# Optimization experiments

Measured on AMD Instinct MI355X. Metric: run time of the kernel, lower is better.

## Reference

```python
import jax, jax.numpy as jnp
import numpy as np

K = 4        # maximum_fertility + 1
OOV_ID = 1
HIDDEN = 512


def setup_inputs() -> dict:
    key = jax.random.key(0)
    ks = jax.random.split(key, 8)
    B, S, D, E, H, V = 4, 128, 512, 256, HIDDEN, 32000
    return {
        "embedded_input": jax.random.normal(ks[0], (B, S, D), jnp.float32),
        "input_mask": jnp.ones((B, S), jnp.int32),
        "emb_table": jax.random.normal(ks[1], (V, E), jnp.float32) * 0.02,
        "W_ih": jax.random.normal(ks[2], (4 * H, D + E), jnp.float32) * 0.02,
        "b_ih": jax.random.normal(ks[3], (4 * H,), jnp.float32) * 0.02,
        "W_hh": jax.random.normal(ks[4], (4 * H, H), jnp.float32) * 0.02,
        "b_hh": jax.random.normal(ks[5], (4 * H,), jnp.float32) * 0.02,
        "W_out": jax.random.normal(ks[6], (V, H), jnp.float32) * 0.02,
        "b_out": jax.random.normal(ks[7], (V,), jnp.float32) * 0.02,
    }


def reference(embedded_input, input_mask, emb_table, W_ih, b_ih, W_hh, b_hh, W_out, b_out):
    B, S, D = embedded_input.shape
    V, E = emb_table.shape
    H = HIDDEN
    N = B * S
    x = embedded_input.reshape(N, D)                      # (N, D)
    h0 = jnp.zeros((N, H), embedded_input.dtype)
    c0 = jnp.zeros((N, H), embedded_input.dtype)
    # initial last_output: one-hot at OOV id (prob mass 1.0 on oov)
    last0 = jnp.zeros((N, V), embedded_input.dtype).at[:, OOV_ID].set(1.0)

    def step(carry, _):
        h, c, last = carry
        # embedding_bag soft mix over full vocab == weighted sum == matmul
        emb_last = last @ emb_table                        # (N, E)
        inp = jnp.concatenate([x, emb_last], axis=1)       # (N, D+E)
        gates = inp @ W_ih.T + b_ih + h @ W_hh.T + b_hh    # (N, 4H)
        i, f, g, o = jnp.split(gates, 4, axis=1)           # torch LSTMCell gate order
        i = jax.nn.sigmoid(i)
        f = jax.nn.sigmoid(f)
        g = jnp.tanh(g)
        o = jax.nn.sigmoid(o)
        c_new = f * c + i * g
        h_new = o * jnp.tanh(c_new)
        # dropout=0 / eval -> dropout mask is all ones (no-op)
        logits = h_new @ W_out.T + b_out                   # (N, V)
        logp = jax.nn.log_softmax(logits, axis=-1)
        return (h_new, c_new, jnp.exp(logp)), logp

    _, outs = jax.lax.scan(step, (h0, c0, last0), None, length=K)  # (K, N, V)
    return outs.transpose(1, 0, 2).reshape(B, S, K, V)
```

## Files before the change

### kernel.cpp

```cpp
#include <hip/hip_runtime.h>
#include <hip/hip_bf16.h>
#include <math.h>

#define N_ROWS 512
#define D_IN   512
#define E_EMB  256
#define H_DIM  512
#define G_DIM  2048
#define V_DIM  32000
#define IN_LD  1280
#define K_STEPS 4
#define OOV_ID 1
#define TBK 64
#define EMB_SPLIT 50
#define EMB_CHUNK 640
#define SEGSTRIDE 512

typedef __attribute__((ext_vector_type(4))) float f32x4;
typedef __attribute__((ext_vector_type(8))) short bf16x8;
typedef __attribute__((ext_vector_type(8))) _Float16 f16x8;

__device__ inline short f2b(float v) {
    __hip_bfloat16 h = __float2bfloat16(v);
    return *reinterpret_cast<short*>(&h);
}

__device__ inline void gload_lds(const short* g, short* l) {
    __builtin_amdgcn_global_load_lds(
        (const __attribute__((address_space(1))) void*)g,
        (__attribute__((address_space(3))) void*)l, 16, 0, 0);
}

template<int TBM, int TBN, int WR_, int WC_, int MODE>
__global__ __launch_bounds__(WR_ * WC_ * 64) void k_gemm(
    const short* __restrict__ A, int lda,
    const short* __restrict__ B, int ldb,
    const float* __restrict__ bias,
    float* __restrict__ C, size_t ldc, int Kc,
    float2* __restrict__ stats,
    float* __restrict__ cstate, short* __restrict__ hdst,
    float* __restrict__ outdst, size_t ldout, const float* __restrict__ lsep)
{
    constexpr int NW = WR_ * WC_;
    constexpr int WMT = TBM / WR_, WNT = TBN / WC_;
    constexpr int WM = WMT / 16, WN = WNT / 16;
    __shared__ short As[TBM * 64];
    __shared__ short Bs[TBN * 64];
    const int tid = threadIdx.x;
    const int lane = tid & 63, wid = tid >> 6;
    const int wr = wid % WR_, wc = wid / WR_;
    const int quad = lane >> 4, l16 = lane & 15;
    const int m0 = blockIdx.y * TBM, n0 = blockIdx.x * TBN;
    const int kbase = blockIdx.z * Kc;
    const int lrow = lane >> 3;
    const int lsw  = ((lane & 7) ^ lrow) * 8;

    f32x4 acc[WM][WN];
#pragma unroll
    for (int i = 0; i < WM; ++i)
#pragma unroll
        for (int j = 0; j < WN; ++j)
#pragma unroll
            for (int r = 0; r < 4; ++r) acc[i][j][r] = 0.0f;

    for (int kt = 0; kt < Kc; kt += TBK) {
        const int k0 = kbase + kt;
        if constexpr (MODE == 5) {
#pragma unroll
            for (int ch = wid; ch < TBN / 8; ch += NW)
                gload_lds(&B[(size_t)(n0 + ch * 8 + lrow) * ldb + k0 + lsw], &Bs[ch * 512]);
            const _Float16* Z = (const _Float16*)A;
#pragma unroll
            for (int ch = wid; ch < TBM / 8; ch += NW) {
                const int row = m0 + ch * 8 + lrow;
                const int col = k0 + lsw;
                f16x8 zv = *(const f16x8*)&Z[(size_t)row * lda + col];
                const float l = lsep[row];
                float lp[8];
#pragma unroll
                for (int q = 0; q < 8; ++q) lp[q] = (float)zv[q] - l;
                float4* od = (float4*)&outdst[(size_t)row * ldout + col];
                od[0] = make_float4(lp[0], lp[1], lp[2], lp[3]);
                od[1] = make_float4(lp[4], lp[5], lp[6], lp[7]);
                bf16x8 p;
#pragma unroll
                for (int q = 0; q < 8; ++q) p[q] = f2b(__expf(lp[q]));
                *(bf16x8*)&As[ch * 512 + lane * 8] = p;
            }
        } else {
#pragma unroll
            for (int ch = wid; ch < TBM / 8; ch += NW)
                gload_lds(&A[(size_t)(m0 + ch * 8 + lrow) * lda + k0 + lsw], &As[ch * 512]);
#pragma unroll
            for (int ch = wid; ch < TBN / 8; ch += NW)
                gload_lds(&B[(size_t)(n0 + ch * 8 + lrow) * ldb + k0 + lsw], &Bs[ch * 512]);
        }
        __syncthreads();
#pragma unroll
        for (int ks = 0; ks < 2; ++ks) {
            bf16x8 af[WM], bfv[WN];
#pragma unroll
            for (int i = 0; i < WM; ++i) {
                int rr = wr * WMT + i * 16 + l16;
                af[i] = *(const bf16x8*)&As[rr * 64 + (((ks * 4 + quad) ^ (l16 & 7)) * 8)];
            }
#pragma unroll
            for (int j = 0; j < WN; ++j) {
                int rr = wc * WNT + j * 16 + l16;
                bfv[j] = *(const bf16x8*)&Bs[rr * 64 + (((ks * 4 + quad) ^ (l16 & 7)) * 8)];
            }
#pragma unroll
            for (int i = 0; i < WM; ++i)
#pragma unroll
                for (int j = 0; j < WN; ++j)
                    acc[i][j] = __builtin_amdgcn_mfma_f32_16x16x32_bf16(af[i], bfv[j], acc[i][j], 0, 0, 0);
        }
        __syncthreads();
    }

    if constexpr (MODE == 3 || MODE == 5) {
        float* Cp = C + (size_t)blockIdx.z * N_ROWS * ldc;
#pragma unroll
        for (int i = 0; i < WM; ++i)
#pragma unroll
            for (int j = 0; j < WN; ++j) {
                const int n = n0 + wc * WNT + j * 16 + l16;
#pragma unroll
                for (int r = 0; r < 4; ++r) {
                    const int m = m0 + wr * WMT + i * 16 + quad * 4 + r;
                    Cp[(size_t)m * ldc + n] = acc[i][j][r];
                }
            }
    } else if constexpr (MODE == 2) {
        float bv[WN];
#pragma unroll
        for (int j = 0; j < WN; ++j) bv[j] = bias[n0 + j * 16 + l16];
        const int jj = (n0 >> 2) + l16;
#pragma unroll
        for (int i = 0; i < WM; ++i) {
#pragma unroll
            for (int r = 0; r < 4; ++r) {
                const int m = m0 + wr * WMT + i * 16 + quad * 4 + r;
                float gi = acc[i][0][r] + bv[0];
                float gf = acc[i][1][r] + bv[1];
                float gg = acc[i][2][r] + bv[2];
                float go = acc[i][3][r] + bv[3];
                float i_ = 1.0f / (1.0f + expf(-gi));
                float f_ = 1.0f / (1.0f + expf(-gf));
                float g_ = tanhf(gg);
                float o_ = 1.0f / (1.0f + expf(-go));
                const size_t ci = (size_t)m * H_DIM + jj;
                float cn = f_ * cstate[ci] + i_ * g_;
                cstate[ci] = cn;
                hdst[(size_t)m * IN_LD + (D_IN + E_EMB) + jj] = f2b(o_ * tanhf(cn));
            }
        }
    } else if constexpr (MODE == 4) {
        _Float16* Ch = (_Float16*)C;
        float bv[WN];
#pragma unroll
        for (int j = 0; j < WN; ++j) bv[j] = bias[n0 + wc * WNT + j * 16 + l16];
#pragma unroll
        for (int i = 0; i < WM; ++i) {
            float rm[4] = {-1e30f, -1e30f, -1e30f, -1e30f};
            float rs[4] = {0.f, 0.f, 0.f, 0.f};
#pragma unroll
            for (int j = 0; j < WN; ++j)
#pragma unroll
                for (int r = 0; r < 4; ++r)
                    rm[r] = fmaxf(rm[r], acc[i][j][r] + bv[j]);
#pragma unroll
            for (int j = 0; j < WN; ++j) {
                const int n = n0 + wc * WNT + j * 16 + l16;
#pragma unroll
                for (int r = 0; r < 4; ++r) {
                    const int m = m0 + wr * WMT + i * 16 + quad * 4 + r;
                    float z = acc[i][j][r] + bv[j];
                    rs[r] += __expf(z - rm[r]);
                    Ch[(size_t)m * ldc + n] = (_Float16)z;
                }
            }
#pragma unroll
            for (int mask = 1; mask < 16; mask <<= 1) {
#pragma unroll
                for (int r = 0; r < 4; ++r) {
                    float om = __shfl_xor(rm[r], mask);
                    float os = __shfl_xor(rs[r], mask);
                    float nm = fmaxf(rm[r], om);
                    rs[r] = rs[r] * __expf(rm[r] - nm) + os * __expf(om - nm);
                    rm[r] = nm;
                }
            }
            if (l16 == 0) {
                const int seg = (n0 + wc * WNT) >> 6;
#pragma unroll
                for (int r = 0; r < 4; ++r) {
                    const int m = m0 + wr * WMT + i * 16 + quad * 4 + r;
                    stats[(size_t)m * SEGSTRIDE + seg] = make_float2(rm[r], rs[r]);
                }
            }
        }
    } else {
        float bv[WN];
#pragma unroll
        for (int j = 0; j < WN; ++j) bv[j] = bias[n0 + wc * WNT + j * 16 + l16];
#pragma unroll
        for (int i = 0; i < WM; ++i)
#pragma unroll
            for (int j = 0; j < WN; ++j) {
                const int n = n0 + wc * WNT + j * 16 + l16;
#pragma unroll
                for (int r = 0; r < 4; ++r) {
                    const int m = m0 + wr * WMT + i * 16 + quad * 4 + r;
                    C[(size_t)m * ldc + n] = acc[i][j][r] + bv[j];
                }
            }
    }
}

__global__ __launch_bounds__(256) void k_prep(
    const float* __restrict__ x, const float* __restrict__ emb_table,
    const float* __restrict__ W_ih, const float* __restrict__ W_hh,
    const float* __restrict__ b_ih, const float* __restrict__ b_hh,
    const float* __restrict__ W_out,
    short* __restrict__ Abuf, short* __restrict__ Wg, float* __restrict__ bsum,
    short* __restrict__ Wout16, float* __restrict__ c)
{
    const int idx0 = blockIdx.x * 256 + threadIdx.x;
    const int gs = gridDim.x * 256;
    const float4* W4 = (const float4*)W_out;
    for (int i = idx0; i < V_DIM * H_DIM / 4; i += gs) {
        float4 v = W4[i];
        short4 o;
        o.x = f2b(v.x); o.y = f2b(v.y); o.z = f2b(v.z); o.w = f2b(v.w);
        ((short4*)Wout16)[i] = o;
    }
    for (int i = idx0; i < G_DIM * IN_LD; i += gs) {
        int rp = i / IN_LD, k = i - rp * IN_LD;
        int j = ((rp >> 6) << 4) | (rp & 15);
        int gate = (rp >> 4) & 3;
        int g = gate * H_DIM + j;
        float v = (k < D_IN + E_EMB) ? W_ih[(size_t)g * (D_IN + E_EMB) + k]
                                     : W_hh[(size_t)g * H_DIM + (k - (D_IN + E_EMB))];
        Wg[i] = f2b(v);
    }
    for (int i = idx0; i < G_DIM; i += gs) {
        int j = ((i >> 6) << 4) | (i & 15);
        int gate = (i >> 4) & 3;
        int g = gate * H_DIM + j;
        bsum[i] = b_ih[g] + b_hh[g];
    }
    for (int i = idx0; i < N_ROWS * IN_LD; i += gs) {
        int n = i / IN_LD, col = i - n * IN_LD;
        float v;
        if (col < D_IN)              v = x[(size_t)n * D_IN + col];
        else if (col < D_IN + E_EMB) v = emb_table[(size_t)OOV_ID * E_EMB + (col - D_IN)];
        else                         v = 0.0f;
        Abuf[i] = f2b(v);
    }
    for (int i = idx0; i < N_ROWS * H_DIM; i += gs) c[i] = 0.0f;
}

__global__ __launch_bounds__(256) void k_trans(const float* __restrict__ emb,
                                               short* __restrict__ embT)
{
    __shared__ float tile[64][65];
    const int v0 = blockIdx.x * 64, e0 = blockIdx.y * 64;
    const int tid = threadIdx.x;
#pragma unroll
    for (int i = 0; i < 16; ++i) {
        int idx = tid + i * 256;
        int vr = idx >> 6, ec = idx & 63;
        tile[vr][ec] = emb[(size_t)(v0 + vr) * E_EMB + e0 + ec];
    }
    __syncthreads();
#pragma unroll
    for (int i = 0; i < 16; ++i) {
        int idx = tid + i * 256;
        int er = idx >> 6, vc = idx & 63;
        embT[(size_t)(e0 + er) * V_DIM + v0 + vc] = f2b(tile[vc][er]);
    }
}

__global__ __launch_bounds__(256) void k_embred(const float* __restrict__ ep,
                                                short* __restrict__ Abuf)
{
    int idx = blockIdx.x * 256 + threadIdx.x;
    int n = idx >> 8, e = idx & 255;
    float s0 = 0.f, s1 = 0.f;
#pragma unroll 2
    for (int z = 0; z < EMB_SPLIT; z += 2) {
        s0 += ep[((size_t)z * N_ROWS + n) * E_EMB + e];
        s1 += ep[((size_t)(z + 1) * N_ROWS + n) * E_EMB + e];
    }
    Abuf[(size_t)n * IN_LD + D_IN + e] = f2b(s0 + s1);
}

__global__ __launch_bounds__(256) void k_lse(const float2* __restrict__ stats,
                                             float* __restrict__ lse)
{
    const int tid = threadIdx.x;
    const int lane = tid & 63, wid = tid >> 6;
    const int n = blockIdx.x * 4 + wid;

    float m = -1e30f, s = 0.0f;
    for (int sg = lane; sg < V_DIM / 64; sg += 64) {
        float2 p = stats[(size_t)n * SEGSTRIDE + sg];
        float nm = fmaxf(m, p.x);
        s = s * __expf(m - nm) + p.y * __expf(p.x - nm);
        m = nm;
    }
#pragma unroll
    for (int mask = 32; mask > 0; mask >>= 1) {
        float om = __shfl_xor(m, mask);
        float os = __shfl_xor(s, mask);
        float nm = fmaxf(m, om);
        s = s * __expf(m - nm) + os * __expf(om - nm);
        m = nm;
    }
    if (lane == 0) lse[n] = m + __logf(s);
}

__global__ __launch_bounds__(256) void k_finish(const _Float16* __restrict__ zbuf,
                                                float* __restrict__ out,
                                                const float* __restrict__ lse,
                                                int step)
{
    const int n = blockIdx.y;
    const float l = lse[n];
    const f16x8* zr = (const f16x8*)(zbuf + (size_t)n * V_DIM);
    float4* row4 = (float4*)(out + ((size_t)n * K_STEPS + step) * V_DIM);
#pragma unroll
    for (int it = 0; it < 2; ++it) {
        const int slot = threadIdx.x + it * 256;
        if (slot < 500) {
            const int cidx = blockIdx.x * 500 + slot;
            f16x8 zv = zr[cidx];
            float lp[8];
#pragma unroll
            for (int k = 0; k < 8; ++k) lp[k] = (float)zv[k] - l;
            row4[cidx * 2]     = make_float4(lp[0], lp[1], lp[2], lp[3]);
            row4[cidx * 2 + 1] = make_float4(lp[4], lp[5], lp[6], lp[7]);
        }
    }
}

extern "C" void kernel_launch(void* const* d_in, const int* in_sizes, int n_in,
                              void* d_out, int out_size, void* d_ws, size_t ws_size,
                              hipStream_t stream) {
    (void)in_sizes; (void)n_in; (void)out_size; (void)ws_size;
    const float* x       = (const float*)d_in[0];
    const float* emb_tab = (const float*)d_in[2];
    const float* W_ih    = (const float*)d_in[3];
    const float* b_ih    = (const float*)d_in[4];
    const float* W_hh    = (const float*)d_in[5];
    const float* b_hh    = (const float*)d_in[6];
    const float* W_out   = (const float*)d_in[7];
    const float* b_out   = (const float*)d_in[8];
    float* out = (float*)d_out;

    char* ws = (char*)d_ws;
    short* Abuf   = (short*)ws;  ws += (size_t)N_ROWS * IN_LD * sizeof(short);
    float* c      = (float*)ws;  ws += (size_t)N_ROWS * H_DIM * sizeof(float);
    short* Wout16 = (short*)ws;  ws += (size_t)V_DIM * H_DIM * sizeof(short);
    short* Wg     = (short*)ws;  ws += (size_t)G_DIM * IN_LD * sizeof(short);
    float* bsum   = (float*)ws;  ws += (size_t)G_DIM * sizeof(float);
    short* embT   = (short*)ws;  ws += (size_t)E_EMB * V_DIM * sizeof(short);
    float2* stats = (float2*)ws; ws += (size_t)N_ROWS * SEGSTRIDE * sizeof(float2);
    float* lse    = (float*)ws;  ws += (size_t)N_ROWS * sizeof(float);
    ws = (char*)(((size_t)ws + 255) & ~(size_t)255);
    _Float16* zbuf = (_Float16*)ws; ws += (size_t)N_ROWS * V_DIM * sizeof(_Float16);
    float* epart   = (float*)ws;    ws += (size_t)EMB_SPLIT * N_ROWS * E_EMB * sizeof(float);

    k_prep<<<2048, 256, 0, stream>>>(x, emb_tab, W_ih, W_hh, b_ih, b_hh, W_out,
                                     Abuf, Wg, bsum, Wout16, c);
    k_trans<<<dim3(V_DIM / 64, E_EMB / 64), 256, 0, stream>>>(emb_tab, embT);

    for (int t = 0; t < K_STEPS; ++t) {
        if (t > 0) {
            k_lse<<<N_ROWS / 4, 256, 0, stream>>>(stats, lse);
            k_gemm<128, 256, 2, 4, 5><<<dim3(1, N_ROWS / 128, EMB_SPLIT), 512, 0, stream>>>(
                (const short*)zbuf, V_DIM, embT, V_DIM, nullptr, epart, E_EMB, EMB_CHUNK,
                nullptr, nullptr, nullptr,
                out + (size_t)(t - 1) * V_DIM, (size_t)K_STEPS * V_DIM, lse);
            k_embred<<<N_ROWS * E_EMB / 256, 256, 0, stream>>>(epart, Abuf);
        }
        k_gemm<64, 64, 4, 1, 2><<<dim3(G_DIM / 64, N_ROWS / 64, 1), 256, 0, stream>>>(
            Abuf, IN_LD, Wg, IN_LD, bsum, nullptr, 0, IN_LD, nullptr, c, Abuf,
            nullptr, 0, nullptr);
        k_gemm<256, 128, 4, 2, 4><<<dim3(V_DIM / 128, N_ROWS / 256, 1), 512, 0, stream>>>(
            Abuf + (D_IN + E_EMB), IN_LD, Wout16, H_DIM, b_out,
            (float*)zbuf, V_DIM, H_DIM, stats, nullptr, nullptr,
            nullptr, 0, nullptr);
    }
    k_lse<<<N_ROWS / 4, 256, 0, stream>>>(stats, lse);
    k_finish<<<dim3(8, N_ROWS), 256, 0, stream>>>(zbuf, out, lse, K_STEPS - 1);
}
```

Measured before the change: 670.3 us.

## Fuse log-sum-exp reduction into output GEMM via last-block ticket; vectorize embred

Removes the separate k_lse launches by having the last-finishing block of each row-tile of the vocab GEMM (detected with an atomic ticket counter) reduce the per-segment max/sum stats into lse. A ticket array is added to the workspace and zeroed in k_prep. k_embred is also rewritten to load float4 and store four bf16 values per thread. This saves kernel launches and the global round trip through lse, but adds atomics, threadfences and a serialized tail reduction in one block per row-tile.

```diff
diff --git a/kernel.cpp b/kernel.cpp
--- a/kernel.cpp
+++ b/kernel.cpp
@@ -200,6 +200,41 @@
                 }
             }
         }
+        int* tick = (int*)hdst;
+        float* lseout = cstate;
+        __threadfence();
+        __shared__ int lastFlag;
+        if (tid == 0)
+            lastFlag = (atomicAdd(&tick[blockIdx.y], 1) == (int)gridDim.x - 1);
+        __syncthreads();
+        if (lastFlag) {
+            if (tid == 0) atomicExch(&tick[blockIdx.y], 0);
+            __threadfence();
+            float2* pm = (float2*)As;
+            const int n = m0 + (tid & (TBM - 1));
+            const int half = tid / TBM;
+            float fm2[2] = {-1e30f, -1e30f}, fs2[2] = {0.f, 0.f};
+            const int sgbase = half * 250;
+            for (int sg = sgbase; sg < sgbase + 250; sg += 2) {
+#pragma unroll
+                for (int q = 0; q < 2; ++q) {
+                    float2 p = stats[(size_t)n * SEGSTRIDE + sg + q];
+                    float nm = fmaxf(fm2[q], p.x);
+                    fs2[q] = fs2[q] * __expf(fm2[q] - nm) + p.y * __expf(p.x - nm);
+                    fm2[q] = nm;
+                }
+            }
+            float M1 = fmaxf(fm2[0], fm2[1]);
+            float S1 = fs2[0] * __expf(fm2[0] - M1) + fs2[1] * __expf(fm2[1] - M1);
+            pm[tid] = make_float2(M1, S1);
+            __syncthreads();
+            if (half == 0) {
+                float2 a = pm[tid], b = pm[tid + TBM];
+                float M = fmaxf(a.x, b.x);
+                float S = a.y * __expf(a.x - M) + b.y * __expf(b.x - M);
+                lseout[n] = M + __logf(S);
+            }
+        }
     } else {
         float bv[WN];
 #pragma unroll
@@ -224,10 +259,11 @@
     const float* __restrict__ b_ih, const float* __restrict__ b_hh,
     const float* __restrict__ W_out,
     short* __restrict__ Abuf, short* __restrict__ Wg, float* __restrict__ bsum,
-    short* __restrict__ Wout16, float* __restrict__ c)
+    short* __restrict__ Wout16, float* __restrict__ c, int* __restrict__ ticket)
 {
     const int idx0 = blockIdx.x * 256 + threadIdx.x;
     const int gs = gridDim.x * 256;
+    if (idx0 < 4) ticket[idx0] = 0;
     const float4* W4 = (const float4*)W_out;
     for (int i = idx0; i < V_DIM * H_DIM / 4; i += gs) {
         float4 v = W4[i];
@@ -286,39 +322,20 @@
                                                 short* __restrict__ Abuf)
 {
     int idx = blockIdx.x * 256 + threadIdx.x;
-    int n = idx >> 8, e = idx & 255;
-    float s0 = 0.f, s1 = 0.f;
+    int n = idx >> 6, e4 = idx & 63;
+    const float4* ep4 = (const float4*)ep;
+    float4 s0 = make_float4(0.f, 0.f, 0.f, 0.f), s1 = s0;
 #pragma unroll 2
     for (int z = 0; z < EMB_SPLIT; z += 2) {
-        s0 += ep[((size_t)z * N_ROWS + n) * E_EMB + e];
-        s1 += ep[((size_t)(z + 1) * N_ROWS + n) * E_EMB + e];
-    }
-    Abuf[(size_t)n * IN_LD + D_IN + e] = f2b(s0 + s1);
-}
-
-__global__ __launch_bounds__(256) void k_lse(const float2* __restrict__ stats,
-                                             float* __restrict__ lse)
-{
-    const int tid = threadIdx.x;
-    const int lane = tid & 63, wid = tid >> 6;
-    const int n = blockIdx.x * 4 + wid;
-
-    float m = -1e30f, s = 0.0f;
-    for (int sg = lane; sg < V_DIM / 64; sg += 64) {
-        float2 p = stats[(size_t)n * SEGSTRIDE + sg];
-        float nm = fmaxf(m, p.x);
-        s = s * __expf(m - nm) + p.y * __expf(p.x - nm);
-        m = nm;
-    }
-#pragma unroll
-    for (int mask = 32; mask > 0; mask >>= 1) {
-        float om = __shfl_xor(m, mask);
-        float os = __shfl_xor(s, mask);
-        float nm = fmaxf(m, om);
-        s = s * __expf(m - nm) + os * __expf(om - nm);
-        m = nm;
-    }
-    if (lane == 0) lse[n] = m + __logf(s);
+        float4 a = ep4[(((size_t)z * N_ROWS + n) * E_EMB >> 2) + e4];
+        float4 b = ep4[(((size_t)(z + 1) * N_ROWS + n) * E_EMB >> 2) + e4];
+        s0.x += a.x; s0.y += a.y; s0.z += a.z; s0.w += a.w;
+        s1.x += b.x; s1.y += b.y; s1.z += b.z; s1.w += b.w;
+    }
+    short4 o;
+    o.x = f2b(s0.x + s1.x); o.y = f2b(s0.y + s1.y);
+    o.z = f2b(s0.z + s1.z); o.w = f2b(s0.w + s1.w);
+    *(short4*)&Abuf[(size_t)n * IN_LD + D_IN + e4 * 4] = o;
 }
 
 __global__ __launch_bounds__(256) void k_finish(const _Float16* __restrict__ zbuf,
@@ -368,31 +385,30 @@
     short* embT   = (short*)ws;  ws += (size_t)E_EMB * V_DIM * sizeof(short);
     float2* stats = (float2*)ws; ws += (size_t)N_ROWS * SEGSTRIDE * sizeof(float2);
     float* lse    = (float*)ws;  ws += (size_t)N_ROWS * sizeof(float);
+    int* ticket   = (int*)ws;    ws += 256;
     ws = (char*)(((size_t)ws + 255) & ~(size_t)255);
     _Float16* zbuf = (_Float16*)ws; ws += (size_t)N_ROWS * V_DIM * sizeof(_Float16);
     float* epart   = (float*)ws;    ws += (size_t)EMB_SPLIT * N_ROWS * E_EMB * sizeof(float);
 
     k_prep<<<2048, 256, 0, stream>>>(x, emb_tab, W_ih, W_hh, b_ih, b_hh, W_out,
-                                     Abuf, Wg, bsum, Wout16, c);
+                                     Abuf, Wg, bsum, Wout16, c, ticket);
     k_trans<<<dim3(V_DIM / 64, E_EMB / 64), 256, 0, stream>>>(emb_tab, embT);
 
     for (int t = 0; t < K_STEPS; ++t) {
         if (t > 0) {
-            k_lse<<<N_ROWS / 4, 256, 0, stream>>>(stats, lse);
             k_gemm<128, 256, 2, 4, 5><<<dim3(1, N_ROWS / 128, EMB_SPLIT), 512, 0, stream>>>(
                 (const short*)zbuf, V_DIM, embT, V_DIM, nullptr, epart, E_EMB, EMB_CHUNK,
                 nullptr, nullptr, nullptr,
                 out + (size_t)(t - 1) * V_DIM, (size_t)K_STEPS * V_DIM, lse);
-            k_embred<<<N_ROWS * E_EMB / 256, 256, 0, stream>>>(epart, Abuf);
+            k_embred<<<N_ROWS * E_EMB / 4 / 256, 256, 0, stream>>>(epart, Abuf);
         }
         k_gemm<64, 64, 4, 1, 2><<<dim3(G_DIM / 64, N_ROWS / 64, 1), 256, 0, stream>>>(
             Abuf, IN_LD, Wg, IN_LD, bsum, nullptr, 0, IN_LD, nullptr, c, Abuf,
             nullptr, 0, nullptr);
         k_gemm<256, 128, 4, 2, 4><<<dim3(V_DIM / 128, N_ROWS / 256, 1), 512, 0, stream>>>(
             Abuf + (D_IN + E_EMB), IN_LD, Wout16, H_DIM, b_out,
-            (float*)zbuf, V_DIM, H_DIM, stats, nullptr, nullptr,
+            (float*)zbuf, V_DIM, H_DIM, stats, lse, (short*)ticket,
             nullptr, 0, nullptr);
     }
-    k_lse<<<N_ROWS / 4, 256, 0, stream>>>(stats, lse);
     k_finish<<<dim3(8, N_ROWS), 256, 0, stream>>>(zbuf, out, lse, K_STEPS - 1);
 }
```

Measured after the change: 1.430 ms. +113.4%, slower.
